# Kernel optimization log

Hardware: AMD Instinct MI355X
Metric: run time of the kernel (lower is better)

Reference implementation:

```python
import jax, jax.numpy as jnp
import numpy as np

ALPHA, BETA, GAMMA, IOU_THR = 1.0, 1.0, 1.0, 0.5


def _smooth_l1(d):
    a = jnp.abs(d)
    return jnp.where(a < 1.0, 0.5 * d * d, a - 0.5)


def setup_inputs() -> dict:
    key = jax.random.key(0)
    ks = jax.random.split(key, 8)
    B, A, G = 16, 120000, 32
    # anchors: valid corner-format boxes on a ~1024px image
    cxy = jax.random.uniform(ks[0], (A, 2), jnp.float32, 0.0, 1024.0)
    wh = jax.random.uniform(ks[1], (A, 2), jnp.float32, 16.0, 256.0)
    anchors = jnp.concatenate([cxy - 0.5 * wh, cxy + 0.5 * wh], axis=-1)  # [A,4]
    # gt boxes: jittered copies of random anchors (guarantees some IoU>=0.5 matches)
    gidx = jax.random.randint(ks[2], (B, G), 0, A)
    jitter = jax.random.uniform(ks[3], (B, G, 4), jnp.float32, -2.0, 2.0)
    gt_boxes = anchors[gidx] + jitter  # [B,G,4], w,h stay > 0
    return {
        "pred_cls": jax.random.normal(ks[4], (B, A, 2), jnp.float32),
        "pred_bbox": jax.random.normal(ks[5], (B, A, 4), jnp.float32),
        "pred_landmarks": jax.random.normal(ks[6], (B, A, 10), jnp.float32),
        "anchors": anchors,
        "gt_boxes": gt_boxes,
        "gt_landmarks": jax.random.normal(ks[7], (B, G, 10), jnp.float32),
    }


def reference(pred_cls, pred_bbox, pred_landmarks, anchors, gt_boxes, gt_landmarks):
    B, A, _ = pred_cls.shape
    G = gt_boxes.shape[1]
    # ---- pairwise IoU: anchors [A,4] vs gt_boxes [B,G,4] -> [B,A,G] ----
    a = anchors[None, :, None, :]     # [1,A,1,4]
    g = gt_boxes[:, None, :, :]       # [B,1,G,4]
    iw = jnp.clip(jnp.minimum(a[..., 2], g[..., 2]) - jnp.maximum(a[..., 0], g[..., 0]), 0.0)
    ih = jnp.clip(jnp.minimum(a[..., 3], g[..., 3]) - jnp.maximum(a[..., 1], g[..., 1]), 0.0)
    inter = iw * ih
    area_a = (anchors[:, 2] - anchors[:, 0]) * (anchors[:, 3] - anchors[:, 1])  # [A]
    area_g = (gt_boxes[..., 2] - gt_boxes[..., 0]) * (gt_boxes[..., 3] - gt_boxes[..., 1])  # [B,G]
    iou = inter / (area_a[None, :, None] + area_g[:, None, :] - inter)
    max_iou = iou.max(axis=-1)                 # [B,A]
    matched = iou.argmax(axis=-1)              # [B,A] int
    pos = max_iou >= IOU_THR                   # [B,A] bool
    npos = pos.sum(axis=1).astype(pred_cls.dtype)  # [B]

    # ---- classification: CE against binary target (0/1 class index) ----
    target_cls = pos.astype(jnp.int32)
    logp = jax.nn.log_softmax(pred_cls, axis=-1)  # [B,A,2]
    ce = -jnp.take_along_axis(logp, target_cls[..., None], axis=-1)[..., 0]  # [B,A]
    cls_loss = ce.mean(axis=1).mean()

    # ---- gather matched gt per anchor ----
    midx4 = jnp.broadcast_to(matched[:, :, None], (B, A, 4))
    mboxes = jnp.take_along_axis(gt_boxes, midx4, axis=1)        # [B,A,4]
    midx10 = jnp.broadcast_to(matched[:, :, None], (B, A, 10))
    mldm = jnp.take_along_axis(gt_landmarks, midx10, axis=1)     # [B,A,10]

    aw = anchors[:, 2] - anchors[:, 0]
    ah = anchors[:, 3] - anchors[:, 1]
    acx = anchors[:, 0] + 0.5 * aw
    acy = anchors[:, 1] + 0.5 * ah
    gw = mboxes[..., 2] - mboxes[..., 0]
    gh = mboxes[..., 3] - mboxes[..., 1]
    gcx = mboxes[..., 0] + 0.5 * gw
    gcy = mboxes[..., 1] + 0.5 * gh
    reg_t = jnp.stack([(gcx - acx) / aw, (gcy - acy) / ah,
                       jnp.log(gw / aw), jnp.log(gh / ah)], axis=-1)  # [B,A,4]

    m = pos[..., None].astype(pred_cls.dtype)
    reg_l = (_smooth_l1(pred_bbox - reg_t) * m).sum(axis=(1, 2))       # [B]
    ldm_l = (_smooth_l1(pred_landmarks - mldm) * m).sum(axis=(1, 2))   # [B]
    has = npos > 0
    denom = jnp.maximum(npos, 1.0)
    reg_loss = jnp.where(has, reg_l / (denom * 4.0), 0.0).mean()   # mean SmoothL1 over pos elems, /B
    ldm_loss = jnp.where(has, ldm_l / (denom * 10.0), 0.0).mean()

    total = ALPHA * cls_loss + BETA * reg_loss + GAMMA * ldm_loss
    return (total, cls_loss, reg_loss, ldm_loss)
```

## Files before the change

### kernel.cpp

```cpp
#include <hip/hip_runtime.h>
#include <math.h>

#define AN 120000
#define BN 16
#define GN 32
#define BLK 256
#define NBX ((AN + BLK - 1) / BLK)
#define NBTOT (NBX * BN)

typedef float f16v __attribute__((ext_vector_type(16)));

__device__ __forceinline__ float sl1(float d) {
    float ad = fabsf(d);
    return ad < 1.0f ? 0.5f * d * d : ad - 0.5f;
}

__global__ __launch_bounds__(512) void prelude(const float* __restrict__ gt_boxes,
                                               float* __restrict__ sg3buf) {
    const int t = threadIdx.x;
    float4 box = *(const float4*)(gt_boxes + t * 4);
    sg3buf[t] = (box.z - box.x) * (box.w - box.y) * (1.f / 3.f);
}

__global__ __launch_bounds__(256) void loss_main(
    const float* __restrict__ pred_cls,
    const float* __restrict__ pred_bbox,
    const float* __restrict__ pred_ldm,
    const float* __restrict__ anchors,
    const float* __restrict__ gt_boxes,
    const float* __restrict__ gt_ldm,
    const float* __restrict__ sg3buf,
    float* __restrict__ partial)
{
    __shared__ float4 gtb[GN];
    const int b   = blockIdx.y;
    const int tid = threadIdx.x;
    const int a   = blockIdx.x * BLK + tid;
    const bool val = (a < AN);

    if (tid < GN) gtb[tid] = *(const float4*)(gt_boxes + (b * GN + tid) * 4);

    float4 an4 = make_float4(0.f, 0.f, 0.f, 0.f);
    if (val) an4 = *(const float4*)(anchors + (size_t)a * 4);
    float2 pc = make_float2(0.f, 0.f);
    if (val) pc = *(const float2*)(pred_cls + ((size_t)b * AN + a) * 2);

    const float sa3 = (an4.z - an4.x) * (an4.w - an4.y) * (1.f / 3.f);

    __syncthreads();

    const float* sg3p = sg3buf + b * GN;
    f16v sA, sB;
    asm volatile("s_load_dwordx16 %0, %2, 0x0\n\t"
                 "s_load_dwordx16 %1, %2, 0x40\n\t"
                 "s_waitcnt lgkmcnt(0)"
                 : "=&s"(sA), "=&s"(sB)
                 : "s"(sg3p));

    bool pos = false;
#define IOUT(G, SG3) {                                                      \
        const float4 gb = gtb[(G)];                                         \
        float iw = fmaxf(fminf(an4.z, gb.z) - fmaxf(an4.x, gb.x), 0.f);     \
        float ih = fminf(an4.w, gb.w) - fmaxf(an4.y, gb.y);                 \
        pos = pos | (iw * ih >= sa3 + (SG3)); }
    #pragma unroll
    for (int g = 0; g < 16; ++g) IOUT(g, sA[g]);
    #pragma unroll
    for (int g = 0; g < 16; ++g) IOUT(g + 16, sB[g]);
#undef IOUT

    float ce = 0.f, np = 0.f, rl = 0.f, ll = 0.f;

    if (val) {
        float d = pc.x - pc.y;
        float lse = fmaxf(pc.x, pc.y) + __logf(1.f + __expf(-fabsf(d)));
        ce = lse - (pos ? pc.y : pc.x);

        if (pos) {
            const float sa = (an4.z - an4.x) * (an4.w - an4.y);
            float bi = -1.f, bu = 1.f; int bg = 0;
            #pragma unroll 8
            for (int g = 0; g < GN; ++g) {
                float4 gb = gtb[g];
                float iw = fmaxf(fminf(an4.z, gb.z) - fmaxf(an4.x, gb.x), 0.f);
                float ih = fmaxf(fminf(an4.w, gb.w) - fmaxf(an4.y, gb.y), 0.f);
                float inter = iw * ih;
                float sg = (gb.z - gb.x) * (gb.w - gb.y);
                float uni = sa + sg - inter;
                bool upd = inter * bu > bi * uni;
                bi = upd ? inter : bi;
                bu = upd ? uni   : bu;
                bg = upd ? g     : bg;
            }
            np = 1.f;
            float4 gb = gtb[bg];
            float aw = an4.z - an4.x, ah = an4.w - an4.y;
            float acx = an4.x + 0.5f * aw, acy = an4.y + 0.5f * ah;
            float gw = gb.z - gb.x, gh = gb.w - gb.y;
            float gcx = gb.x + 0.5f * gw, gcy = gb.y + 0.5f * gh;
            float t0 = (gcx - acx) / aw;
            float t1 = (gcy - acy) / ah;
            float t2 = __logf(gw / aw);
            float t3 = __logf(gh / ah);
            const float4 pb = *(const float4*)(pred_bbox + ((size_t)b * AN + a) * 4);
            rl = sl1(pb.x - t0) + sl1(pb.y - t1) + sl1(pb.z - t2) + sl1(pb.w - t3);
            const float* pl = pred_ldm + ((size_t)b * AN + a) * 10;
            const float* gl = gt_ldm + ((size_t)b * GN + bg) * 10;
            float s = 0.f;
            #pragma unroll
            for (int j = 0; j < 10; ++j) s += sl1(pl[j] - gl[j]);
            ll = s;
        }
    }

    __shared__ float red[4][4];
    #pragma unroll
    for (int off = 32; off > 0; off >>= 1) {
        ce += __shfl_down(ce, off, 64);
        np += __shfl_down(np, off, 64);
        rl += __shfl_down(rl, off, 64);
        ll += __shfl_down(ll, off, 64);
    }
    const int lane = tid & 63, wid = tid >> 6;
    if (lane == 0) { red[0][wid] = ce; red[1][wid] = np; red[2][wid] = rl; red[3][wid] = ll; }
    __syncthreads();
    if (tid < 4) {
        float s = red[tid][0] + red[tid][1] + red[tid][2] + red[tid][3];
        partial[(size_t)tid * (BN * NBX) + (size_t)b * NBX + blockIdx.x] = s;
    }
}

__global__ __launch_bounds__(256) void reduce_finalize(
    const float* __restrict__ partial, float* __restrict__ out)
{
    __shared__ float rowsum[64];
    const int tid = threadIdx.x;
    const int row = tid >> 2;
    const int sub = tid & 3;

    float s = 0.f;
    const float* p = partial + (size_t)row * NBX;
    for (int j = sub; j < NBX; j += 4) s += p[j];
    s += __shfl_down(s, 1, 64);
    s += __shfl_down(s, 2, 64);
    if (sub == 0) rowsum[row] = s;
    __syncthreads();

    if (tid == 0) {
        float cls = 0.f, reg = 0.f, ldm = 0.f;
        for (int b = 0; b < BN; ++b) {
            cls += rowsum[0 * BN + b] / (float)AN;
            float npv = rowsum[1 * BN + b];
            float den = fmaxf(npv, 1.f);
            bool has = npv > 0.f;
            reg += has ? rowsum[2 * BN + b] / (den * 4.f)  : 0.f;
            ldm += has ? rowsum[3 * BN + b] / (den * 10.f) : 0.f;
        }
        cls /= (float)BN; reg /= (float)BN; ldm /= (float)BN;
        out[0] = cls + reg + ldm;
        out[1] = cls;
        out[2] = reg;
        out[3] = ldm;
    }
}

extern "C" void kernel_launch(void* const* d_in, const int* in_sizes, int n_in,
                              void* d_out, int out_size, void* d_ws, size_t ws_size,
                              hipStream_t stream) {
    const float* pred_cls  = (const float*)d_in[0];
    const float* pred_bbox = (const float*)d_in[1];
    const float* pred_ldm  = (const float*)d_in[2];
    const float* anchors   = (const float*)d_in[3];
    const float* gt_boxes  = (const float*)d_in[4];
    const float* gt_ldm    = (const float*)d_in[5];
    float* out = (float*)d_out;

    float* sg3buf  = (float*)d_ws;
    float* partial = (float*)((char*)d_ws + 2048);

    prelude<<<1, 512, 0, stream>>>(gt_boxes, sg3buf);
    dim3 grid(NBX, BN);
    loss_main<<<grid, BLK, 0, stream>>>(pred_cls, pred_bbox, pred_ldm, anchors,
                                        gt_boxes, gt_ldm, sg3buf, partial);
    reduce_finalize<<<1, 256, 0, stream>>>(partial, out);
}
```

Measured before the change: 219.9 us.

## Process four anchors per thread with software-prefetched anchor and class loads

Each thread now handles four anchors strided by the block size instead of one, so the grid shrinks fourfold. The anchor box and class logits for the next anchor are loaded before the current one is processed, overlapping memory latency with the IoU compute. Per-block overhead (gt box shared load, scalar loads, block reduction, partial writes) is amortised over more work. The cost is more registers per thread and less parallelism: about 118 blocks per batch, 1888 in total.

```diff
diff --git a/kernel.cpp b/kernel.cpp
--- a/kernel.cpp
+++ b/kernel.cpp
@@ -5,8 +5,9 @@
 #define BN 16
 #define GN 32
 #define BLK 256
-#define NBX ((AN + BLK - 1) / BLK)
-#define NBTOT (NBX * BN)
+#define TPB 4
+#define TILE (BLK * TPB)
+#define NBX ((AN + TILE - 1) / TILE)
 
 typedef float f16v __attribute__((ext_vector_type(16)));
 
@@ -35,17 +36,18 @@
     __shared__ float4 gtb[GN];
     const int b   = blockIdx.y;
     const int tid = threadIdx.x;
-    const int a   = blockIdx.x * BLK + tid;
-    const bool val = (a < AN);
+    const int base = blockIdx.x * TILE + tid;
 
     if (tid < GN) gtb[tid] = *(const float4*)(gt_boxes + (b * GN + tid) * 4);
 
-    float4 an4 = make_float4(0.f, 0.f, 0.f, 0.f);
-    if (val) an4 = *(const float4*)(anchors + (size_t)a * 4);
-    float2 pc = make_float2(0.f, 0.f);
-    if (val) pc = *(const float2*)(pred_cls + ((size_t)b * AN + a) * 2);
-
-    const float sa3 = (an4.z - an4.x) * (an4.w - an4.y) * (1.f / 3.f);
+    int a0 = base;
+    bool val0 = (a0 < AN);
+    float4 an_cur = make_float4(0.f, 0.f, 0.f, 0.f);
+    float2 pc_cur = make_float2(0.f, 0.f);
+    if (val0) {
+        an_cur = *(const float4*)(anchors + (size_t)a0 * 4);
+        pc_cur = *(const float2*)(pred_cls + ((size_t)b * AN + a0) * 2);
+    }
 
     __syncthreads();
 
@@ -57,59 +59,80 @@
                  : "=&s"(sA), "=&s"(sB)
                  : "s"(sg3p));
 
-    bool pos = false;
+    float ce = 0.f, np = 0.f, rl = 0.f, ll = 0.f;
+
+    #pragma unroll
+    for (int t = 0; t < TPB; ++t) {
+        const int a = base + t * BLK;
+        const bool val = (a < AN);
+        const float4 an4 = an_cur;
+        const float2 pc  = pc_cur;
+
+        if (t + 1 < TPB) {
+            const int an_ = base + (t + 1) * BLK;
+            if (an_ < AN) {
+                an_cur = *(const float4*)(anchors + (size_t)an_ * 4);
+                pc_cur = *(const float2*)(pred_cls + ((size_t)b * AN + an_) * 2);
+            } else {
+                an_cur = make_float4(0.f, 0.f, 0.f, 0.f);
+                pc_cur = make_float2(0.f, 0.f);
+            }
+        }
+
+        const float sa3 = (an4.z - an4.x) * (an4.w - an4.y) * (1.f / 3.f);
+
+        bool pos = false;
 #define IOUT(G, SG3) {                                                      \
         const float4 gb = gtb[(G)];                                         \
         float iw = fmaxf(fminf(an4.z, gb.z) - fmaxf(an4.x, gb.x), 0.f);     \
         float ih = fminf(an4.w, gb.w) - fmaxf(an4.y, gb.y);                 \
         pos = pos | (iw * ih >= sa3 + (SG3)); }
-    #pragma unroll
-    for (int g = 0; g < 16; ++g) IOUT(g, sA[g]);
-    #pragma unroll
-    for (int g = 0; g < 16; ++g) IOUT(g + 16, sB[g]);
+        #pragma unroll
+        for (int g = 0; g < 16; ++g) IOUT(g, sA[g]);
+        #pragma unroll
+        for (int g = 0; g < 16; ++g) IOUT(g + 16, sB[g]);
 #undef IOUT
 
-    float ce = 0.f, np = 0.f, rl = 0.f, ll = 0.f;
-
-    if (val) {
-        float d = pc.x - pc.y;
-        float lse = fmaxf(pc.x, pc.y) + __logf(1.f + __expf(-fabsf(d)));
-        ce = lse - (pos ? pc.y : pc.x);
-
-        if (pos) {
-            const float sa = (an4.z - an4.x) * (an4.w - an4.y);
-            float bi = -1.f, bu = 1.f; int bg = 0;
-            #pragma unroll 8
-            for (int g = 0; g < GN; ++g) {
-                float4 gb = gtb[g];
-                float iw = fmaxf(fminf(an4.z, gb.z) - fmaxf(an4.x, gb.x), 0.f);
-                float ih = fmaxf(fminf(an4.w, gb.w) - fmaxf(an4.y, gb.y), 0.f);
-                float inter = iw * ih;
-                float sg = (gb.z - gb.x) * (gb.w - gb.y);
-                float uni = sa + sg - inter;
-                bool upd = inter * bu > bi * uni;
-                bi = upd ? inter : bi;
-                bu = upd ? uni   : bu;
-                bg = upd ? g     : bg;
+        if (val) {
+            float d = pc.x - pc.y;
+            float lse = fmaxf(pc.x, pc.y) + __logf(1.f + __expf(-fabsf(d)));
+            ce += lse - (pos ? pc.y : pc.x);
+
+            if (pos) {
+                const float sa = (an4.z - an4.x) * (an4.w - an4.y);
+                float bi = -1.f, bu = 1.f; int bg = 0;
+                #pragma unroll 8
+                for (int g = 0; g < GN; ++g) {
+                    float4 gb = gtb[g];
+                    float iw = fmaxf(fminf(an4.z, gb.z) - fmaxf(an4.x, gb.x), 0.f);
+                    float ih = fmaxf(fminf(an4.w, gb.w) - fmaxf(an4.y, gb.y), 0.f);
+                    float inter = iw * ih;
+                    float sg = (gb.z - gb.x) * (gb.w - gb.y);
+                    float uni = sa + sg - inter;
+                    bool upd = inter * bu > bi * uni;
+                    bi = upd ? inter : bi;
+                    bu = upd ? uni   : bu;
+                    bg = upd ? g     : bg;
+                }
+                np += 1.f;
+                float4 gb = gtb[bg];
+                float aw = an4.z - an4.x, ah = an4.w - an4.y;
+                float acx = an4.x + 0.5f * aw, acy = an4.y + 0.5f * ah;
+                float gw = gb.z - gb.x, gh = gb.w - gb.y;
+                float gcx = gb.x + 0.5f * gw, gcy = gb.y + 0.5f * gh;
+                float t0 = (gcx - acx) / aw;
+                float t1 = (gcy - acy) / ah;
+                float t2 = __logf(gw / aw);
+                float t3 = __logf(gh / ah);
+                const float4 pb = *(const float4*)(pred_bbox + ((size_t)b * AN + a) * 4);
+                rl += sl1(pb.x - t0) + sl1(pb.y - t1) + sl1(pb.z - t2) + sl1(pb.w - t3);
+                const float* pl = pred_ldm + ((size_t)b * AN + a) * 10;
+                const float* gl = gt_ldm + ((size_t)b * GN + bg) * 10;
+                float s = 0.f;
+                #pragma unroll
+                for (int j = 0; j < 10; ++j) s += sl1(pl[j] - gl[j]);
+                ll += s;
             }
-            np = 1.f;
-            float4 gb = gtb[bg];
-            float aw = an4.z - an4.x, ah = an4.w - an4.y;
-            float acx = an4.x + 0.5f * aw, acy = an4.y + 0.5f * ah;
-            float gw = gb.z - gb.x, gh = gb.w - gb.y;
-            float gcx = gb.x + 0.5f * gw, gcy = gb.y + 0.5f * gh;
-            float t0 = (gcx - acx) / aw;
-            float t1 = (gcy - acy) / ah;
-            float t2 = __logf(gw / aw);
-            float t3 = __logf(gh / ah);
-            const float4 pb = *(const float4*)(pred_bbox + ((size_t)b * AN + a) * 4);
-            rl = sl1(pb.x - t0) + sl1(pb.y - t1) + sl1(pb.z - t2) + sl1(pb.w - t3);
-            const float* pl = pred_ldm + ((size_t)b * AN + a) * 10;
-            const float* gl = gt_ldm + ((size_t)b * GN + bg) * 10;
-            float s = 0.f;
-            #pragma unroll
-            for (int j = 0; j < 10; ++j) s += sl1(pl[j] - gl[j]);
-            ll = s;
         }
     }
 
```

Result: faster. 209.0 us (-5.0%).
